# Kernel optimization log

Hardware: AMD Instinct MI355X
Metric: run time of the kernel (lower is better)

Reference implementation:

```python
import jax, jax.numpy as jnp
import numpy as np

O_FEATURES = 4096
I_FEATURES = 4096
N_TOKENS = 8192


def _unpack_int4(packed, out_shape):
    # packed: int32 holding uint8 byte values; two signed int4 per byte (offset-8)
    p = packed.astype(jnp.int32)
    even = (p & 15) - 8          # low nibble
    odd = ((p >> 4) & 15) - 8    # high nibble
    # interleave: stacked[0::2] = even, stacked[1::2] = odd
    stacked = jnp.stack([even, odd], axis=-1).reshape(-1)
    return stacked.reshape(out_shape)


def setup_inputs() -> dict:
    key = jax.random.key(0)
    k1, k2, k3 = jax.random.split(key, 3)
    x = jax.random.normal(k1, (N_TOKENS, I_FEATURES), dtype=jnp.float32)
    packed_w = jax.random.randint(k2, (O_FEATURES * I_FEATURES // 2,), 0, 256, dtype=jnp.int32)
    # per-output-channel scale (positive, as produced by abs-max / qmax)
    scale = jax.random.uniform(k3, (O_FEATURES, 1), dtype=jnp.float32) * 0.01 + 1e-4
    return {"x": x, "packed_w": packed_w, "scale": scale}


def reference(x, packed_w, scale):
    # dequantize: unpack int4 -> target dtype, multiply per-row scale
    int_w = _unpack_int4(packed_w, (O_FEATURES, I_FEATURES)).astype(x.dtype)  # [O, I]
    w = int_w * scale.astype(x.dtype)  # scale broadcasts [O,1] over [O,I]
    # downstream quantized linear: y = x @ W^T
    return jnp.einsum('ni,oi->no', x, w)
```

## Files before the change

kernel.cpp:

```cpp
#include <hip/hip_runtime.h>

typedef unsigned char u8;
typedef signed char s8;
typedef unsigned int u32;
typedef __attribute__((ext_vector_type(4))) int i32x4;

#define M_TOK 8192
#define N_OUT 4096
#define K_IN  4096
#define NT    32

static __device__ __forceinline__ u32 pack4(float4 v, float inv) {
    int q0 = __float2int_rn(v.x * inv) & 255;
    int q1 = __float2int_rn(v.y * inv) & 255;
    int q2 = __float2int_rn(v.z * inv) & 255;
    int q3 = __float2int_rn(v.w * inv) & 255;
    return (u32)q0 | ((u32)q1 << 8) | ((u32)q2 << 16) | ((u32)q3 << 24);
}

__global__ __launch_bounds__(256) void prep_kernel(const float* __restrict__ x,
                                                   const int* __restrict__ pw,
                                                   s8* __restrict__ xq,
                                                   float* __restrict__ sx,
                                                   s8* __restrict__ wq) {
    __shared__ float red[4];
    int bid = blockIdx.x;
    int t = threadIdx.x;
    if (bid < M_TOK) {
        int row = bid;
        const float4* xr = (const float4*)(x + (size_t)row * K_IN);
        float4 v0 = xr[t], v1 = xr[t + 256], v2 = xr[t + 512], v3 = xr[t + 768];
        float am = 0.f;
        am = fmaxf(am, fmaxf(fmaxf(fabsf(v0.x), fabsf(v0.y)), fmaxf(fabsf(v0.z), fabsf(v0.w))));
        am = fmaxf(am, fmaxf(fmaxf(fabsf(v1.x), fabsf(v1.y)), fmaxf(fabsf(v1.z), fabsf(v1.w))));
        am = fmaxf(am, fmaxf(fmaxf(fabsf(v2.x), fabsf(v2.y)), fmaxf(fabsf(v2.z), fabsf(v2.w))));
        am = fmaxf(am, fmaxf(fmaxf(fabsf(v3.x), fabsf(v3.y)), fmaxf(fabsf(v3.z), fabsf(v3.w))));
#pragma unroll
        for (int o = 32; o > 0; o >>= 1) am = fmaxf(am, __shfl_xor(am, o));
        if ((t & 63) == 0) red[t >> 6] = am;
        __syncthreads();
        am = fmaxf(fmaxf(red[0], red[1]), fmaxf(red[2], red[3]));
        float inv = (am > 0.f) ? 127.f / am : 0.f;
        if (t == 0) sx[row] = (am > 0.f) ? am / 127.f : 0.f;
        u32* out = (u32*)(xq + (size_t)row * K_IN);
        out[t]       = pack4(v0, inv);
        out[t + 256] = pack4(v1, inv);
        out[t + 512] = pack4(v2, inv);
        out[t + 768] = pack4(v3, inv);
    } else {
        const int n4 = (N_OUT * K_IN / 2) / 4;
        int idx = (bid - M_TOK) * 256 + t;
        const int stride = 512 * 256;
        for (int i = idx; i < n4; i += stride) {
            int4 p = *(const int4*)(pw + (size_t)i * 4);
            u32 lo = (u32)(((p.x & 15) - 8) & 255)
                   | ((u32)((((p.x >> 4) & 15) - 8) & 255) << 8)
                   | ((u32)((((p.y) & 15) - 8) & 255) << 16)
                   | ((u32)((((p.y >> 4) & 15) - 8) & 255) << 24);
            u32 hi = (u32)(((p.z & 15) - 8) & 255)
                   | ((u32)((((p.z >> 4) & 15) - 8) & 255) << 8)
                   | ((u32)((((p.w) & 15) - 8) & 255) << 16)
                   | ((u32)((((p.w >> 4) & 15) - 8) & 255) << 24);
            uint2 o; o.x = lo; o.y = hi;
            *(uint2*)(wq + (size_t)i * 8) = o;
        }
    }
}

#define MFMA(a, b, c) __builtin_amdgcn_mfma_i32_16x16x64_i8(a, b, c, 0, 0, 0)

static __device__ __forceinline__ i32x4 ldsv(const u8* p, int idx) {
    return *(const i32x4*)(p + idx);
}

#define MFMA16(A00, A01, A10, A11, M0, M1)                \
    acc[M0][0] = MFMA(A00, b00, acc[M0][0]);              \
    acc[M0][1] = MFMA(A00, b10, acc[M0][1]);              \
    acc[M0][2] = MFMA(A00, b20, acc[M0][2]);              \
    acc[M0][3] = MFMA(A00, b30, acc[M0][3]);              \
    acc[M1][0] = MFMA(A10, b00, acc[M1][0]);              \
    acc[M1][1] = MFMA(A10, b10, acc[M1][1]);              \
    acc[M1][2] = MFMA(A10, b20, acc[M1][2]);              \
    acc[M1][3] = MFMA(A10, b30, acc[M1][3]);              \
    acc[M0][0] = MFMA(A01, b01, acc[M0][0]);              \
    acc[M0][1] = MFMA(A01, b11, acc[M0][1]);              \
    acc[M0][2] = MFMA(A01, b21, acc[M0][2]);              \
    acc[M0][3] = MFMA(A01, b31, acc[M0][3]);              \
    acc[M1][0] = MFMA(A11, b01, acc[M1][0]);              \
    acc[M1][1] = MFMA(A11, b11, acc[M1][1]);              \
    acc[M1][2] = MFMA(A11, b21, acc[M1][2]);              \
    acc[M1][3] = MFMA(A11, b31, acc[M1][3]);

__global__ __launch_bounds__(512, 2) void gemmra_i8_kernel(const s8* __restrict__ A,
                                                           const s8* __restrict__ B,
                                                           const float* __restrict__ sx,
                                                           const float* __restrict__ scale,
                                                           float* __restrict__ C) {
    __shared__ __align__(16) u8 lds[131072];

#define GLo(src, dstIdx)                                                        \
    __builtin_amdgcn_global_load_lds(                                           \
        (const __attribute__((address_space(1))) void*)(src),                   \
        (__attribute__((address_space(3))) void*)&lds[dstIdx], 16, 0, 0)

    int wg = blockIdx.x;
    int swz = (wg & 7) * 64 + (wg >> 3);
    int bm = swz >> 4;
    int bn = swz & 15;

    int t = threadIdx.x;
    int l = t & 63;
    int wid = t >> 6;
    int wr = wid >> 2;
    int wc = wid & 3;

    const size_t soff = (size_t)(t >> 3) * K_IN + (size_t)((((t & 7) ^ ((t >> 3) & 7)) << 4));
    const size_t S64 = (size_t)64 * K_IN;
    const int t16 = t * 16;

    const s8* Alo = A + (size_t)(bm * 256) * K_IN;
    const s8* Ahi = Alo + (size_t)128 * K_IN;
    const s8* Blo = B + (size_t)(bn * 256) * K_IN;
    const s8* Bhi = Blo + (size_t)128 * K_IN;

    const int kx = (l & 7) << 4;
    const int koff0 = (((l >> 4) << 4)) ^ kx;
    const int koff1 = koff0 ^ 64;
    const int aB = wr * 16384 + (l & 15) * 128;
    const int bB = 32768 + wc * 8192 + (l & 15) * 128;

    i32x4 acc[8][4] = {};

    GLo(Blo + soff, 32768 + t16);         GLo(Blo + soff + S64, 32768 + t16 + 8192);
    GLo(Bhi + soff, 49152 + t16);         GLo(Bhi + soff + S64, 49152 + t16 + 8192);
    GLo(Alo + soff, t16);                 GLo(Alo + soff + S64, t16 + 8192);
    GLo(Ahi + soff, 16384 + t16);         GLo(Ahi + soff + S64, 16384 + t16 + 8192);
    GLo(Blo + soff + 128, 98304 + t16);   GLo(Blo + soff + S64 + 128, 98304 + t16 + 8192);
    GLo(Bhi + soff + 128, 114688 + t16);  GLo(Bhi + soff + S64 + 128, 114688 + t16 + 8192);
    asm volatile("s_waitcnt vmcnt(4)" ::: "memory");
    __builtin_amdgcn_s_barrier();

    for (int T = 0; T < NT; ++T) {
        const int buf = T & 1;
        const u8* L = lds + buf * 65536;

        i32x4 b00 = ldsv(L, bB + koff0),        b01 = ldsv(L, bB + koff1);
        i32x4 b10 = ldsv(L, bB + 2048 + koff0), b11 = ldsv(L, bB + 2048 + koff1);
        i32x4 b20 = ldsv(L, bB + 4096 + koff0), b21 = ldsv(L, bB + 4096 + koff1);
        i32x4 b30 = ldsv(L, bB + 6144 + koff0), b31 = ldsv(L, bB + 6144 + koff1);
        i32x4 p00 = ldsv(L, aB + koff0),        p01 = ldsv(L, aB + koff1);
        i32x4 p10 = ldsv(L, aB + 2048 + koff0), p11 = ldsv(L, aB + 2048 + koff1);

        if (T + 1 < NT) {
            size_t ko = (size_t)(T + 1) * 128;
            int d = (buf ^ 1) * 65536 + t16;
            GLo(Alo + soff + ko, d);                 GLo(Alo + soff + S64 + ko, d + 8192);
            GLo(Ahi + soff + ko, d + 16384);         GLo(Ahi + soff + S64 + ko, d + 24576);
        }

        i32x4 q00 = ldsv(L, aB + 4096 + koff0), q01 = ldsv(L, aB + 4096 + koff1);
        i32x4 q10 = ldsv(L, aB + 6144 + koff0), q11 = ldsv(L, aB + 6144 + koff1);

        __builtin_amdgcn_s_setprio(1);
        MFMA16(p00, p01, p10, p11, 0, 1);
        __builtin_amdgcn_s_setprio(0);

        p00 = ldsv(L, aB + 8192 + koff0);  p01 = ldsv(L, aB + 8192 + koff1);
        p10 = ldsv(L, aB + 10240 + koff0); p11 = ldsv(L, aB + 10240 + koff1);

        __builtin_amdgcn_s_setprio(1);
        MFMA16(q00, q01, q10, q11, 2, 3);
        __builtin_amdgcn_s_setprio(0);

        __builtin_amdgcn_s_barrier();
        asm volatile("" ::: "memory");

        if (T + 2 < NT) {
            size_t ko = (size_t)(T + 2) * 128;
            int d = buf * 65536 + 32768 + t16;
            GLo(Blo + soff + ko, d);          GLo(Blo + soff + S64 + ko, d + 8192);
            GLo(Bhi + soff + ko, d + 16384);  GLo(Bhi + soff + S64 + ko, d + 24576);
        }

        q00 = ldsv(L, aB + 12288 + koff0); q01 = ldsv(L, aB + 12288 + koff1);
        q10 = ldsv(L, aB + 14336 + koff0); q11 = ldsv(L, aB + 14336 + koff1);

        __builtin_amdgcn_s_setprio(1);
        MFMA16(p00, p01, p10, p11, 4, 5);
        MFMA16(q00, q01, q10, q11, 6, 7);
        __builtin_amdgcn_s_setprio(0);

        if (T < NT - 2) asm volatile("s_waitcnt vmcnt(4)" ::: "memory");
        else            asm volatile("s_waitcnt vmcnt(0)" ::: "memory");
        __builtin_amdgcn_s_barrier();
    }

    int col0 = bn * 256 + wc * 64 + (l & 15);
    float sc_[4];
#pragma unroll
    for (int n = 0; n < 4; ++n) sc_[n] = scale[col0 + n * 16];

#pragma unroll
    for (int m = 0; m < 8; ++m) {
        int row0 = bm * 256 + wr * 128 + m * 16 + (l >> 4) * 4;
        float4 sxr = *(const float4*)(sx + row0);
        float sxa[4] = {sxr.x, sxr.y, sxr.z, sxr.w};
#pragma unroll
        for (int n = 0; n < 4; ++n) {
            int gcol = col0 + n * 16;
#pragma unroll
            for (int j = 0; j < 4; ++j)
                C[(size_t)(row0 + j) * N_OUT + gcol] = (float)acc[m][n][j] * sxa[j] * sc_[n];
        }
    }
#undef GLo
}

__global__ __launch_bounds__(256) void gemm_fb_kernel(const float* __restrict__ X,
                                                      const int* __restrict__ PW,
                                                      const float* __restrict__ S,
                                                      float* __restrict__ C) {
    __shared__ float sxm[64][33];
    __shared__ float swm[64][33];
    int bm = blockIdx.x / (N_OUT / 64);
    int bn = blockIdx.x % (N_OUT / 64);
    int t = threadIdx.x;
    int r = t >> 2, c8 = (t & 3) * 8;
    int tx = t & 15, ty = t >> 4;
    float acc[4][4] = {};
    for (int k0 = 0; k0 < K_IN; k0 += 32) {
        const float* xs = X + (size_t)(bm * 64 + r) * K_IN + k0 + c8;
#pragma unroll
        for (int j = 0; j < 8; ++j) sxm[r][c8 + j] = xs[j];
        const int* ps = PW + ((size_t)(bn * 64 + r) * K_IN + k0 + c8) / 2;
#pragma unroll
        for (int j = 0; j < 4; ++j) {
            int b = ps[j];
            swm[r][c8 + 2 * j]     = (float)((b & 15) - 8);
            swm[r][c8 + 2 * j + 1] = (float)(((b >> 4) & 15) - 8);
        }
        __syncthreads();
#pragma unroll
        for (int kk = 0; kk < 32; ++kk) {
            float a[4], w[4];
#pragma unroll
            for (int i = 0; i < 4; ++i) a[i] = sxm[ty * 4 + i][kk];
#pragma unroll
            for (int j = 0; j < 4; ++j) w[j] = swm[tx * 4 + j][kk];
#pragma unroll
            for (int i = 0; i < 4; ++i)
#pragma unroll
                for (int j = 0; j < 4; ++j) acc[i][j] += a[i] * w[j];
        }
        __syncthreads();
    }
#pragma unroll
    for (int i = 0; i < 4; ++i) {
        int gr = bm * 64 + ty * 4 + i;
#pragma unroll
        for (int j = 0; j < 4; ++j) {
            int gc = bn * 64 + tx * 4 + j;
            C[(size_t)gr * N_OUT + gc] = acc[i][j] * S[gc];
        }
    }
}

extern "C" void kernel_launch(void* const* d_in, const int* in_sizes, int n_in,
                              void* d_out, int out_size, void* d_ws, size_t ws_size,
                              hipStream_t stream) {
    const float* x  = (const float*)d_in[0];
    const int*   pw = (const int*)d_in[1];
    const float* sc = (const float*)d_in[2];
    float* out = (float*)d_out;

    const size_t xq_bytes = (size_t)M_TOK * K_IN;
    const size_t wq_bytes = (size_t)N_OUT * K_IN;
    const size_t sx_bytes = (size_t)M_TOK * sizeof(float);
    const size_t need = xq_bytes + wq_bytes + sx_bytes;

    if (ws_size >= need) {
        s8* xq = (s8*)d_ws;
        s8* wq = xq + xq_bytes;
        float* sx = (float*)(wq + wq_bytes);
        prep_kernel<<<dim3(M_TOK + 512), dim3(256), 0, stream>>>(x, pw, xq, sx, wq);
        gemmra_i8_kernel<<<dim3((M_TOK / 256) * (N_OUT / 256)), dim3(512), 0, stream>>>(
            xq, wq, sx, sc, out);
    } else {
        gemm_fb_kernel<<<dim3((M_TOK / 64) * (N_OUT / 64)), dim3(256), 0, stream>>>(x, pw, sc, out);
    }
}
```

Before: 170.8 us.

## Restructure int8 GEMM to 128x256 tiles with three-stage LDS pipeline

Replaces the 256x256-tile, K=128, double-buffered int8 MFMA GEMM with a 128x256 tile, K=64 per step, using a three-stage ring buffer in LDS (72 KB instead of 128 KB). Launch bounds go from 2 to 4 blocks per CU, the grid doubles, and the grid swizzle and LDS swizzle are adjusted. The aim is more occupancy and deeper prefetch to hide global-load latency. In exchange, each tile reuses data less, per-step MFMA work is smaller and barriers are more frequent.

```diff
diff --git a/kernel.cpp b/kernel.cpp
--- a/kernel.cpp
+++ b/kernel.cpp
@@ -8,7 +8,7 @@
 #define M_TOK 8192
 #define N_OUT 4096
 #define K_IN  4096
-#define NT    32
+#define NT    64
 
 static __device__ __forceinline__ u32 pack4(float4 v, float inv) {
     int q0 = __float2int_rn(v.x * inv) & 255;
@@ -73,30 +73,12 @@
     return *(const i32x4*)(p + idx);
 }
 
-#define MFMA16(A00, A01, A10, A11, M0, M1)                \
-    acc[M0][0] = MFMA(A00, b00, acc[M0][0]);              \
-    acc[M0][1] = MFMA(A00, b10, acc[M0][1]);              \
-    acc[M0][2] = MFMA(A00, b20, acc[M0][2]);              \
-    acc[M0][3] = MFMA(A00, b30, acc[M0][3]);              \
-    acc[M1][0] = MFMA(A10, b00, acc[M1][0]);              \
-    acc[M1][1] = MFMA(A10, b10, acc[M1][1]);              \
-    acc[M1][2] = MFMA(A10, b20, acc[M1][2]);              \
-    acc[M1][3] = MFMA(A10, b30, acc[M1][3]);              \
-    acc[M0][0] = MFMA(A01, b01, acc[M0][0]);              \
-    acc[M0][1] = MFMA(A01, b11, acc[M0][1]);              \
-    acc[M0][2] = MFMA(A01, b21, acc[M0][2]);              \
-    acc[M0][3] = MFMA(A01, b31, acc[M0][3]);              \
-    acc[M1][0] = MFMA(A11, b01, acc[M1][0]);              \
-    acc[M1][1] = MFMA(A11, b11, acc[M1][1]);              \
-    acc[M1][2] = MFMA(A11, b21, acc[M1][2]);              \
-    acc[M1][3] = MFMA(A11, b31, acc[M1][3]);
-
-__global__ __launch_bounds__(512, 2) void gemmra_i8_kernel(const s8* __restrict__ A,
+__global__ __launch_bounds__(512, 4) void gemm3b_i8_kernel(const s8* __restrict__ A,
                                                            const s8* __restrict__ B,
                                                            const float* __restrict__ sx,
                                                            const float* __restrict__ scale,
                                                            float* __restrict__ C) {
-    __shared__ __align__(16) u8 lds[131072];
+    __shared__ __align__(16) u8 lds[73728];
 
 #define GLo(src, dstIdx)                                                        \
     __builtin_amdgcn_global_load_lds(                                           \
@@ -104,7 +86,7 @@
         (__attribute__((address_space(3))) void*)&lds[dstIdx], 16, 0, 0)
 
     int wg = blockIdx.x;
-    int swz = (wg & 7) * 64 + (wg >> 3);
+    int swz = (wg & 7) * 128 + (wg >> 3);
     int bm = swz >> 4;
     int bn = swz & 15;
 
@@ -114,85 +96,68 @@
     int wr = wid >> 2;
     int wc = wid & 3;
 
-    const size_t soff = (size_t)(t >> 3) * K_IN + (size_t)((((t & 7) ^ ((t >> 3) & 7)) << 4));
-    const size_t S64 = (size_t)64 * K_IN;
+    const size_t soff = (size_t)(t >> 2) * K_IN + (size_t)((((t & 3) ^ ((t >> 3) & 3)) << 4));
+    const size_t S128 = (size_t)128 * K_IN;
     const int t16 = t * 16;
 
-    const s8* Alo = A + (size_t)(bm * 256) * K_IN;
-    const s8* Ahi = Alo + (size_t)128 * K_IN;
-    const s8* Blo = B + (size_t)(bn * 256) * K_IN;
-    const s8* Bhi = Blo + (size_t)128 * K_IN;
-
-    const int kx = (l & 7) << 4;
-    const int koff0 = (((l >> 4) << 4)) ^ kx;
-    const int koff1 = koff0 ^ 64;
-    const int aB = wr * 16384 + (l & 15) * 128;
-    const int bB = 32768 + wc * 8192 + (l & 15) * 128;
-
-    i32x4 acc[8][4] = {};
-
-    GLo(Blo + soff, 32768 + t16);         GLo(Blo + soff + S64, 32768 + t16 + 8192);
-    GLo(Bhi + soff, 49152 + t16);         GLo(Bhi + soff + S64, 49152 + t16 + 8192);
-    GLo(Alo + soff, t16);                 GLo(Alo + soff + S64, t16 + 8192);
-    GLo(Ahi + soff, 16384 + t16);         GLo(Ahi + soff + S64, 16384 + t16 + 8192);
-    GLo(Blo + soff + 128, 98304 + t16);   GLo(Blo + soff + S64 + 128, 98304 + t16 + 8192);
-    GLo(Bhi + soff + 128, 114688 + t16);  GLo(Bhi + soff + S64 + 128, 114688 + t16 + 8192);
-    asm volatile("s_waitcnt vmcnt(4)" ::: "memory");
+    const s8* Ablk = A + (size_t)(bm * 128) * K_IN;
+    const s8* Bblk = B + (size_t)(bn * 256) * K_IN;
+
+    const int ksw = (((l >> 4) ^ ((l >> 1) & 3)) << 4);
+    const int aL = wr * 4096 + (l & 15) * 64 + ksw;
+    const int bL = 8192 + wc * 4096 + (l & 15) * 64 + ksw;
+
+    i32x4 acc[4][4] = {};
+
+#define STAGE(DB, TT) do {                                          \
+        size_t ko = (size_t)(TT) * 64;                              \
+        GLo(Ablk + soff + ko,        (DB) + t16);                   \
+        GLo(Bblk + soff + ko,        (DB) + 8192 + t16);            \
+        GLo(Bblk + soff + S128 + ko, (DB) + 16384 + t16);           \
+    } while (0)
+
+    STAGE(0, 0);
+    STAGE(24576, 1);
+    asm volatile("s_waitcnt vmcnt(3)" ::: "memory");
     __builtin_amdgcn_s_barrier();
 
+    int cur = 0, stg = 2 * 24576;
     for (int T = 0; T < NT; ++T) {
-        const int buf = T & 1;
-        const u8* L = lds + buf * 65536;
-
-        i32x4 b00 = ldsv(L, bB + koff0),        b01 = ldsv(L, bB + koff1);
-        i32x4 b10 = ldsv(L, bB + 2048 + koff0), b11 = ldsv(L, bB + 2048 + koff1);
-        i32x4 b20 = ldsv(L, bB + 4096 + koff0), b21 = ldsv(L, bB + 4096 + koff1);
-        i32x4 b30 = ldsv(L, bB + 6144 + koff0), b31 = ldsv(L, bB + 6144 + koff1);
-        i32x4 p00 = ldsv(L, aB + koff0),        p01 = ldsv(L, aB + koff1);
-        i32x4 p10 = ldsv(L, aB + 2048 + koff0), p11 = ldsv(L, aB + 2048 + koff1);
-
-        if (T + 1 < NT) {
-            size_t ko = (size_t)(T + 1) * 128;
-            int d = (buf ^ 1) * 65536 + t16;
-            GLo(Alo + soff + ko, d);                 GLo(Alo + soff + S64 + ko, d + 8192);
-            GLo(Ahi + soff + ko, d + 16384);         GLo(Ahi + soff + S64 + ko, d + 24576);
-        }
-
-        i32x4 q00 = ldsv(L, aB + 4096 + koff0), q01 = ldsv(L, aB + 4096 + koff1);
-        i32x4 q10 = ldsv(L, aB + 6144 + koff0), q11 = ldsv(L, aB + 6144 + koff1);
+        const u8* L = lds + cur;
+
+        if (T + 2 < NT) STAGE(stg, T + 2);
+
+        i32x4 b0 = ldsv(L, bL),        b1 = ldsv(L, bL + 1024);
+        i32x4 b2 = ldsv(L, bL + 2048), b3 = ldsv(L, bL + 3072);
+        i32x4 a0 = ldsv(L, aL),        a1 = ldsv(L, aL + 1024);
+        i32x4 a2 = ldsv(L, aL + 2048), a3 = ldsv(L, aL + 3072);
 
         __builtin_amdgcn_s_setprio(1);
-        MFMA16(p00, p01, p10, p11, 0, 1);
+        acc[0][0] = MFMA(a0, b0, acc[0][0]);
+        acc[0][1] = MFMA(a0, b1, acc[0][1]);
+        acc[0][2] = MFMA(a0, b2, acc[0][2]);
+        acc[0][3] = MFMA(a0, b3, acc[0][3]);
+        acc[1][0] = MFMA(a1, b0, acc[1][0]);
+        acc[1][1] = MFMA(a1, b1, acc[1][1]);
+        acc[1][2] = MFMA(a1, b2, acc[1][2]);
+        acc[1][3] = MFMA(a1, b3, acc[1][3]);
+        acc[2][0] = MFMA(a2, b0, acc[2][0]);
+        acc[2][1] = MFMA(a2, b1, acc[2][1]);
+        acc[2][2] = MFMA(a2, b2, acc[2][2]);
+        acc[2][3] = MFMA(a2, b3, acc[2][3]);
+        acc[3][0] = MFMA(a3, b0, acc[3][0]);
+        acc[3][1] = MFMA(a3, b1, acc[3][1]);
+        acc[3][2] = MFMA(a3, b2, acc[3][2]);
+        acc[3][3] = MFMA(a3, b3, acc[3][3]);
         __builtin_amdgcn_s_setprio(0);
 
-        p00 = ldsv(L, aB + 8192 + koff0);  p01 = ldsv(L, aB + 8192 + koff1);
-        p10 = ldsv(L, aB + 10240 + koff0); p11 = ldsv(L, aB + 10240 + koff1);
-
-        __builtin_amdgcn_s_setprio(1);
-        MFMA16(q00, q01, q10, q11, 2, 3);
-        __builtin_amdgcn_s_setprio(0);
-
+        if (T + 2 < NT)      asm volatile("s_waitcnt vmcnt(3)" ::: "memory");
+        else if (T + 1 < NT) asm volatile("s_waitcnt vmcnt(0)" ::: "memory");
         __builtin_amdgcn_s_barrier();
-        asm volatile("" ::: "memory");
-
-        if (T + 2 < NT) {
-            size_t ko = (size_t)(T + 2) * 128;
-            int d = buf * 65536 + 32768 + t16;
-            GLo(Blo + soff + ko, d);          GLo(Blo + soff + S64 + ko, d + 8192);
-            GLo(Bhi + soff + ko, d + 16384);  GLo(Bhi + soff + S64 + ko, d + 24576);
-        }
-
-        q00 = ldsv(L, aB + 12288 + koff0); q01 = ldsv(L, aB + 12288 + koff1);
-        q10 = ldsv(L, aB + 14336 + koff0); q11 = ldsv(L, aB + 14336 + koff1);
-
-        __builtin_amdgcn_s_setprio(1);
-        MFMA16(p00, p01, p10, p11, 4, 5);
-        MFMA16(q00, q01, q10, q11, 6, 7);
-        __builtin_amdgcn_s_setprio(0);
-
-        if (T < NT - 2) asm volatile("s_waitcnt vmcnt(4)" ::: "memory");
-        else            asm volatile("s_waitcnt vmcnt(0)" ::: "memory");
-        __builtin_amdgcn_s_barrier();
+
+        int nxt = cur + 24576; if (nxt == 73728) nxt = 0;
+        cur = nxt;
+        stg += 24576; if (stg == 73728) stg = 0;
     }
 
     int col0 = bn * 256 + wc * 64 + (l & 15);
@@ -201,8 +166,8 @@
     for (int n = 0; n < 4; ++n) sc_[n] = scale[col0 + n * 16];
 
 #pragma unroll
-    for (int m = 0; m < 8; ++m) {
-        int row0 = bm * 256 + wr * 128 + m * 16 + (l >> 4) * 4;
+    for (int m = 0; m < 4; ++m) {
+        int row0 = bm * 128 + wr * 64 + m * 16 + (l >> 4) * 4;
         float4 sxr = *(const float4*)(sx + row0);
         float sxa[4] = {sxr.x, sxr.y, sxr.z, sxr.w};
 #pragma unroll
@@ -213,6 +178,7 @@
                 C[(size_t)(row0 + j) * N_OUT + gcol] = (float)acc[m][n][j] * sxa[j] * sc_[n];
         }
     }
+#undef STAGE
 #undef GLo
 }
 
@@ -283,7 +249,7 @@
         s8* wq = xq + xq_bytes;
         float* sx = (float*)(wq + wq_bytes);
         prep_kernel<<<dim3(M_TOK + 512), dim3(256), 0, stream>>>(x, pw, xq, sx, wq);
-        gemmra_i8_kernel<<<dim3((M_TOK / 256) * (N_OUT / 256)), dim3(512), 0, stream>>>(
+        gemm3b_i8_kernel<<<dim3((M_TOK / 128) * (N_OUT / 256)), dim3(512), 0, stream>>>(
             xq, wq, sx, sc, out);
     } else {
         gemm_fb_kernel<<<dim3((M_TOK / 64) * (N_OUT / 64)), dim3(256), 0, stream>>>(x, pw, sc, out);
```

Result: slower. 191.3 us (+12.0%).

## Rotate LDS fragment loads across tiles with ping-pong register sets

Applied to the files above, without the earlier changes.

The K loop is unrolled by two with X/Y register sets. After the end-of-tile barrier, the next tile's B fragments and first A fragments are loaded from LDS before the last MFMA group of the current tile runs, so their latency hides behind compute instead of stalling at the start of each iteration. This raises register pressure (extra 12 i32x4 live values) under a 2-wave-per-SIMD launch bound, which could cause spills.

```diff
diff --git a/kernel.cpp b/kernel.cpp
--- a/kernel.cpp
+++ b/kernel.cpp
@@ -73,29 +73,29 @@
     return *(const i32x4*)(p + idx);
 }
 
-#define MFMA16(A00, A01, A10, A11, M0, M1)                \
-    acc[M0][0] = MFMA(A00, b00, acc[M0][0]);              \
-    acc[M0][1] = MFMA(A00, b10, acc[M0][1]);              \
-    acc[M0][2] = MFMA(A00, b20, acc[M0][2]);              \
-    acc[M0][3] = MFMA(A00, b30, acc[M0][3]);              \
-    acc[M1][0] = MFMA(A10, b00, acc[M1][0]);              \
-    acc[M1][1] = MFMA(A10, b10, acc[M1][1]);              \
-    acc[M1][2] = MFMA(A10, b20, acc[M1][2]);              \
-    acc[M1][3] = MFMA(A10, b30, acc[M1][3]);              \
-    acc[M0][0] = MFMA(A01, b01, acc[M0][0]);              \
-    acc[M0][1] = MFMA(A01, b11, acc[M0][1]);              \
-    acc[M0][2] = MFMA(A01, b21, acc[M0][2]);              \
-    acc[M0][3] = MFMA(A01, b31, acc[M0][3]);              \
-    acc[M1][0] = MFMA(A11, b01, acc[M1][0]);              \
-    acc[M1][1] = MFMA(A11, b11, acc[M1][1]);              \
-    acc[M1][2] = MFMA(A11, b21, acc[M1][2]);              \
-    acc[M1][3] = MFMA(A11, b31, acc[M1][3]);
-
-__global__ __launch_bounds__(512, 2) void gemmra_i8_kernel(const s8* __restrict__ A,
-                                                           const s8* __restrict__ B,
-                                                           const float* __restrict__ sx,
-                                                           const float* __restrict__ scale,
-                                                           float* __restrict__ C) {
+#define MFMA16(A00, A01, A10, A11, M0, M1, BB)            \
+    acc[M0][0] = MFMA(A00, BB[0], acc[M0][0]);            \
+    acc[M0][1] = MFMA(A00, BB[2], acc[M0][1]);            \
+    acc[M0][2] = MFMA(A00, BB[4], acc[M0][2]);            \
+    acc[M0][3] = MFMA(A00, BB[6], acc[M0][3]);            \
+    acc[M1][0] = MFMA(A10, BB[0], acc[M1][0]);            \
+    acc[M1][1] = MFMA(A10, BB[2], acc[M1][1]);            \
+    acc[M1][2] = MFMA(A10, BB[4], acc[M1][2]);            \
+    acc[M1][3] = MFMA(A10, BB[6], acc[M1][3]);            \
+    acc[M0][0] = MFMA(A01, BB[1], acc[M0][0]);            \
+    acc[M0][1] = MFMA(A01, BB[3], acc[M0][1]);            \
+    acc[M0][2] = MFMA(A01, BB[5], acc[M0][2]);            \
+    acc[M0][3] = MFMA(A01, BB[7], acc[M0][3]);            \
+    acc[M1][0] = MFMA(A11, BB[1], acc[M1][0]);            \
+    acc[M1][1] = MFMA(A11, BB[3], acc[M1][1]);            \
+    acc[M1][2] = MFMA(A11, BB[5], acc[M1][2]);            \
+    acc[M1][3] = MFMA(A11, BB[7], acc[M1][3]);
+
+__global__ __launch_bounds__(512, 2) void gemmrot_i8_kernel(const s8* __restrict__ A,
+                                                            const s8* __restrict__ B,
+                                                            const float* __restrict__ sx,
+                                                            const float* __restrict__ scale,
+                                                            float* __restrict__ C) {
     __shared__ __align__(16) u8 lds[131072];
 
 #define GLo(src, dstIdx)                                                        \
@@ -139,61 +139,83 @@
     GLo(Bhi + soff + 128, 114688 + t16);  GLo(Bhi + soff + S64 + 128, 114688 + t16 + 8192);
     asm volatile("s_waitcnt vmcnt(4)" ::: "memory");
     __builtin_amdgcn_s_barrier();
-
-    for (int T = 0; T < NT; ++T) {
-        const int buf = T & 1;
-        const u8* L = lds + buf * 65536;
-
-        i32x4 b00 = ldsv(L, bB + koff0),        b01 = ldsv(L, bB + koff1);
-        i32x4 b10 = ldsv(L, bB + 2048 + koff0), b11 = ldsv(L, bB + 2048 + koff1);
-        i32x4 b20 = ldsv(L, bB + 4096 + koff0), b21 = ldsv(L, bB + 4096 + koff1);
-        i32x4 b30 = ldsv(L, bB + 6144 + koff0), b31 = ldsv(L, bB + 6144 + koff1);
-        i32x4 p00 = ldsv(L, aB + koff0),        p01 = ldsv(L, aB + koff1);
-        i32x4 p10 = ldsv(L, aB + 2048 + koff0), p11 = ldsv(L, aB + 2048 + koff1);
-
-        if (T + 1 < NT) {
-            size_t ko = (size_t)(T + 1) * 128;
-            int d = (buf ^ 1) * 65536 + t16;
-            GLo(Alo + soff + ko, d);                 GLo(Alo + soff + S64 + ko, d + 8192);
-            GLo(Ahi + soff + ko, d + 16384);         GLo(Ahi + soff + S64 + ko, d + 24576);
-        }
-
-        i32x4 q00 = ldsv(L, aB + 4096 + koff0), q01 = ldsv(L, aB + 4096 + koff1);
-        i32x4 q10 = ldsv(L, aB + 6144 + koff0), q11 = ldsv(L, aB + 6144 + koff1);
-
-        __builtin_amdgcn_s_setprio(1);
-        MFMA16(p00, p01, p10, p11, 0, 1);
-        __builtin_amdgcn_s_setprio(0);
-
-        p00 = ldsv(L, aB + 8192 + koff0);  p01 = ldsv(L, aB + 8192 + koff1);
-        p10 = ldsv(L, aB + 10240 + koff0); p11 = ldsv(L, aB + 10240 + koff1);
-
-        __builtin_amdgcn_s_setprio(1);
-        MFMA16(q00, q01, q10, q11, 2, 3);
-        __builtin_amdgcn_s_setprio(0);
-
-        __builtin_amdgcn_s_barrier();
-        asm volatile("" ::: "memory");
-
-        if (T + 2 < NT) {
-            size_t ko = (size_t)(T + 2) * 128;
-            int d = buf * 65536 + 32768 + t16;
-            GLo(Blo + soff + ko, d);          GLo(Blo + soff + S64 + ko, d + 8192);
-            GLo(Bhi + soff + ko, d + 16384);  GLo(Bhi + soff + S64 + ko, d + 24576);
-        }
-
-        q00 = ldsv(L, aB + 12288 + koff0); q01 = ldsv(L, aB + 12288 + koff1);
-        q10 = ldsv(L, aB + 14336 + koff0); q11 = ldsv(L, aB + 14336 + koff1);
-
-        __builtin_amdgcn_s_setprio(1);
-        MFMA16(p00, p01, p10, p11, 4, 5);
-        MFMA16(q00, q01, q10, q11, 6, 7);
-        __builtin_amdgcn_s_setprio(0);
-
-        if (T < NT - 2) asm volatile("s_waitcnt vmcnt(4)" ::: "memory");
-        else            asm volatile("s_waitcnt vmcnt(0)" ::: "memory");
-        __builtin_amdgcn_s_barrier();
-    }
+    asm volatile("" ::: "memory");
+
+    i32x4 bX[8], pX[4], bY[8], pY[4];
+    bX[0] = ldsv(lds, bB + koff0);        bX[1] = ldsv(lds, bB + koff1);
+    bX[2] = ldsv(lds, bB + 2048 + koff0); bX[3] = ldsv(lds, bB + 2048 + koff1);
+    bX[4] = ldsv(lds, bB + 4096 + koff0); bX[5] = ldsv(lds, bB + 4096 + koff1);
+    bX[6] = ldsv(lds, bB + 6144 + koff0); bX[7] = ldsv(lds, bB + 6144 + koff1);
+    pX[0] = ldsv(lds, aB + koff0);        pX[1] = ldsv(lds, aB + koff1);
+    pX[2] = ldsv(lds, aB + 2048 + koff0); pX[3] = ldsv(lds, aB + 2048 + koff1);
+
+#define TILE_BODY(T, Cb, Nb, BC, PC, BN, PN)                                  \
+  do {                                                                        \
+    if ((T) + 1 < NT) {                                                       \
+      size_t ko = (size_t)((T) + 1) * 128;                                    \
+      GLo(Alo + soff + ko,        (Nb) + t16);                                \
+      GLo(Alo + soff + S64 + ko,  (Nb) + 8192 + t16);                         \
+      GLo(Ahi + soff + ko,        (Nb) + 16384 + t16);                        \
+      GLo(Ahi + soff + S64 + ko,  (Nb) + 24576 + t16);                        \
+    }                                                                         \
+    i32x4 q00 = ldsv(lds, (Cb) + aB + 4096 + koff0);                          \
+    i32x4 q01 = ldsv(lds, (Cb) + aB + 4096 + koff1);                          \
+    i32x4 q10 = ldsv(lds, (Cb) + aB + 6144 + koff0);                          \
+    i32x4 q11 = ldsv(lds, (Cb) + aB + 6144 + koff1);                          \
+    __builtin_amdgcn_s_setprio(1);                                            \
+    MFMA16(PC[0], PC[1], PC[2], PC[3], 0, 1, BC);                             \
+    __builtin_amdgcn_s_setprio(0);                                            \
+    i32x4 r00 = ldsv(lds, (Cb) + aB + 8192 + koff0);                          \
+    i32x4 r01 = ldsv(lds, (Cb) + aB + 8192 + koff1);                          \
+    i32x4 r10 = ldsv(lds, (Cb) + aB + 10240 + koff0);                         \
+    i32x4 r11 = ldsv(lds, (Cb) + aB + 10240 + koff1);                         \
+    __builtin_amdgcn_s_setprio(1);                                            \
+    MFMA16(q00, q01, q10, q11, 2, 3, BC);                                     \
+    __builtin_amdgcn_s_setprio(0);                                            \
+    __builtin_amdgcn_s_barrier();                                             \
+    asm volatile("" ::: "memory");                                            \
+    if ((T) + 2 < NT) {                                                       \
+      size_t ko2 = (size_t)((T) + 2) * 128;                                   \
+      GLo(Blo + soff + ko2,       (Cb) + 32768 + t16);                        \
+      GLo(Blo + soff + S64 + ko2, (Cb) + 40960 + t16);                        \
+      GLo(Bhi + soff + ko2,       (Cb) + 49152 + t16);                        \
+      GLo(Bhi + soff + S64 + ko2, (Cb) + 57344 + t16);                        \
+    }                                                                         \
+    i32x4 s00 = ldsv(lds, (Cb) + aB + 12288 + koff0);                         \
+    i32x4 s01 = ldsv(lds, (Cb) + aB + 12288 + koff1);                         \
+    i32x4 s10 = ldsv(lds, (Cb) + aB + 14336 + koff0);                         \
+    i32x4 s11 = ldsv(lds, (Cb) + aB + 14336 + koff1);                         \
+    __builtin_amdgcn_s_setprio(1);                                            \
+    MFMA16(r00, r01, r10, r11, 4, 5, BC);                                     \
+    __builtin_amdgcn_s_setprio(0);                                            \
+    if ((T) < NT - 2) asm volatile("s_waitcnt vmcnt(4)" ::: "memory");        \
+    else              asm volatile("s_waitcnt vmcnt(0)" ::: "memory");        \
+    __builtin_amdgcn_s_barrier();                                             \
+    asm volatile("" ::: "memory");                                            \
+    if ((T) + 1 < NT) {                                                       \
+      BN[0] = ldsv(lds, (Nb) + bB + koff0);                                   \
+      BN[1] = ldsv(lds, (Nb) + bB + koff1);                                   \
+      BN[2] = ldsv(lds, (Nb) + bB + 2048 + koff0);                            \
+      BN[3] = ldsv(lds, (Nb) + bB + 2048 + koff1);                            \
+      BN[4] = ldsv(lds, (Nb) + bB + 4096 + koff0);                            \
+      BN[5] = ldsv(lds, (Nb) + bB + 4096 + koff1);                            \
+      BN[6] = ldsv(lds, (Nb) + bB + 6144 + koff0);                            \
+      BN[7] = ldsv(lds, (Nb) + bB + 6144 + koff1);                            \
+      PN[0] = ldsv(lds, (Nb) + aB + koff0);                                   \
+      PN[1] = ldsv(lds, (Nb) + aB + koff1);                                   \
+      PN[2] = ldsv(lds, (Nb) + aB + 2048 + koff0);                            \
+      PN[3] = ldsv(lds, (Nb) + aB + 2048 + koff1);                            \
+    }                                                                         \
+    __builtin_amdgcn_s_setprio(1);                                            \
+    MFMA16(s00, s01, s10, s11, 6, 7, BC);                                     \
+    __builtin_amdgcn_s_setprio(0);                                            \
+  } while (0)
+
+    for (int T = 0; T < NT; T += 2) {
+        TILE_BODY(T,     0,     65536, bX, pX, bY, pY);
+        TILE_BODY(T + 1, 65536, 0,     bY, pY, bX, pX);
+    }
+#undef TILE_BODY
 
     int col0 = bn * 256 + wc * 64 + (l & 15);
     float sc_[4];
@@ -283,7 +305,7 @@
         s8* wq = xq + xq_bytes;
         float* sx = (float*)(wq + wq_bytes);
         prep_kernel<<<dim3(M_TOK + 512), dim3(256), 0, stream>>>(x, pw, xq, sx, wq);
-        gemmra_i8_kernel<<<dim3((M_TOK / 256) * (N_OUT / 256)), dim3(512), 0, stream>>>(
+        gemmrot_i8_kernel<<<dim3((M_TOK / 256) * (N_OUT / 256)), dim3(512), 0, stream>>>(
             xq, wq, sx, sc, out);
     } else {
         gemm_fb_kernel<<<dim3((M_TOK / 64) * (N_OUT / 64)), dim3(256), 0, stream>>>(x, pw, sc, out);
```

After: 217.8 us. +27.5%, slower.
